# Kernel tuning notes

Measured on AMD Instinct MI355X. Metric: run time of the kernel, lower is better.

The kernel has to match this reference:

```python
import jax, jax.numpy as jnp
import numpy as np
import math

B, S, D, H = 64, 575, 256, 8
FF = 4 * D
EPS = 1e-5
DILATIONS = (1, 2, 4)


def _ln(x, g, b):
    mu = jnp.mean(x, axis=-1, keepdims=True)
    var = jnp.var(x, axis=-1, keepdims=True)
    return (x - mu) * jax.lax.rsqrt(var + EPS) * g + b


def setup_inputs() -> dict:
    key = jax.random.key(0)
    ks = jax.random.split(key, 8)
    w = lambda k, shape: jax.random.normal(k, shape, jnp.float32) * 0.02
    return {
        'state': jax.random.normal(ks[0], (B, S, D), jnp.float32),
        'conv_w': w(ks[1], (3, D, D, 3, 3)),
        'conv_b': jnp.zeros((3, D), jnp.float32),
        'qkv_w': w(ks[2], (3 * D, D)),
        'qkv_b': jnp.zeros((3 * D,), jnp.float32),
        'o_w': w(ks[3], (D, D)),
        'o_b': jnp.zeros((D,), jnp.float32),
        'attn_bias': w(ks[4], (H, S, S)),
        'ffp_w': w(ks[5], (FF, D)),
        'ffp_b': jnp.zeros((FF,), jnp.float32),
        'ffg_w': w(ks[6], (FF, D)),
        'ffg_b': jnp.zeros((FF,), jnp.float32),
        'ffo_w': w(ks[7], (D, FF)),
        'ffo_b': jnp.zeros((D,), jnp.float32),
        'n1_g': jnp.ones((D,), jnp.float32), 'n1_b': jnp.zeros((D,), jnp.float32),
        'n2_g': jnp.ones((D,), jnp.float32), 'n2_b': jnp.zeros((D,), jnp.float32),
        'n3_g': jnp.ones((D,), jnp.float32), 'n3_b': jnp.zeros((D,), jnp.float32),
    }


def _forward(state, conv_w, conv_b, qkv_w, qkv_b, o_w, o_b, attn_bias,
             ffp_w, ffp_b, ffg_w, ffg_b, ffo_w, ffo_b,
             n1_g, n1_b, n2_g, n2_b, n3_g, n3_b):
    b, s, d = state.shape
    h = attn_bias.shape[0]
    hd = d // h
    spatial = int(round(math.sqrt(s + 1)))  # grid_size + 1; spatial^2 == s+1 here

    # --- multi-scale dilated conv mixing ---
    pad = jnp.zeros((b, 1, d), state.dtype)
    h2d = jnp.concatenate([pad, state], axis=1)            # (B, S+1, D)
    h2d = jnp.transpose(h2d, (0, 2, 1)).reshape(b, d, spatial, spatial)
    conv_sum = 0.0
    for i, dil in enumerate(DILATIONS):
        y = jax.lax.conv_general_dilated(
            h2d, conv_w[i], window_strides=(1, 1),
            padding=[(dil, dil), (dil, dil)], rhs_dilation=(dil, dil),
            dimension_numbers=('NCHW', 'OIHW', 'NCHW'))
        conv_sum = conv_sum + y + conv_b[i][None, :, None, None]
    h_flat = jnp.transpose(conv_sum.reshape(b, d, -1), (0, 2, 1))  # (B, S+1, D)
    hmix = h_flat[:, 1:, :]

    state = _ln(state + hmix, n1_g, n1_b)

    # --- self-attention with learned per-head pair bias ---
    qkv = state @ qkv_w.T + qkv_b                          # (B, S, 3D)
    q, k, v = jnp.split(qkv, 3, axis=-1)
    # NOTE: replicate torch's reshape (no transpose): (B,S,D) -> (B,H,S,hd)
    q = q.reshape(b, h, s, hd)
    k = k.reshape(b, h, s, hd)
    v = v.reshape(b, h, s, hd)
    scores = jnp.einsum('bhsd,bhtd->bhst', q, k) / math.sqrt(hd)
    scores = scores + attn_bias[None]
    attn = jax.nn.softmax(scores, axis=-1)
    out = jnp.einsum('bhst,bhtd->bhsd', attn, v)
    out = jnp.transpose(out, (0, 2, 1, 3)).reshape(b, s, d)

    state = _ln(state + out @ o_w.T + o_b, n2_g, n2_b)

    # --- gated feed-forward ---
    proj = state @ ffp_w.T + ffp_b
    gate = jax.nn.sigmoid(state @ ffg_w.T + ffg_b)
    ff = (proj * gate) @ ffo_w.T + ffo_b
    return _ln(state + ff, n3_g, n3_b)


def reference(state, conv_w, conv_b, qkv_w, qkv_b, o_w, o_b, attn_bias,
              ffp_w, ffp_b, ffg_w, ffg_b, ffo_w, ffo_b,
              n1_g, n1_b, n2_g, n2_b, n3_g, n3_b):
    return _forward(state, conv_w, conv_b, qkv_w, qkv_b, o_w, o_b, attn_bias,
                    ffp_w, ffp_b, ffg_w, ffg_b, ffo_w, ffo_b,
                    n1_g, n1_b, n2_g, n2_b, n3_g, n3_b)
```

## Files before the change

kernel.cpp:

```cpp
#include <hip/hip_runtime.h>
#include <hip/hip_bf16.h>
#include <cstdio>


typedef __attribute__((ext_vector_type(8))) short s8v;
typedef __attribute__((ext_vector_type(4))) float f32x4;
typedef unsigned short u16;

constexpr int kB = 64, kS = 575, kD = 256, kH = 8, kP = 576, kFF = 1024;
constexpr int kRows = kB * kS;
constexpr float kEps = 1e-5f;
constexpr float kScale = 0.17677669529663687f;
constexpr size_t kPdStride = 9420800;

__device__ __forceinline__ u16 f2b(float f) {
  __hip_bfloat16 h = __float2bfloat16(f);
  return *reinterpret_cast<u16*>(&h);
}
__device__ __forceinline__ void unpack2(unsigned int w, float& lo, float& hi) {
  union { float f; unsigned int u; } a, b;
  a.u = w << 16;
  b.u = w & 0xffff0000u;
  lo = a.f;
  hi = b.f;
}

__device__ __forceinline__ void gll16(const void* g, void* l) {
  __builtin_amdgcn_global_load_lds((const __attribute__((address_space(1))) void*)g,
                                   (__attribute__((address_space(3))) void*)l, 16, 0, 0);
}

__global__ void k_pack_convw(const float* __restrict__ cw, u16* __restrict__ wc) {
  int idx = blockIdx.x * 256 + threadIdx.x;
  if (idx >= 27 * kD * kD) return;
  int ci = idx & 255;
  int co = (idx >> 8) & 255;
  int tap = idx >> 16;
  int i = tap / 9, r = tap - i * 9;
  int ky = r / 3, kx = r - ky * 3;
  wc[idx] = f2b(cw[(((size_t)(i * kD + co) * kD + ci) * 3 + ky) * 3 + kx]);
}

__global__ void k_tobf16(const float* __restrict__ in, u16* __restrict__ out, int n) {
  int i = blockIdx.x * 256 + threadIdx.x;
  if (i < n) out[i] = f2b(in[i]);
}

__global__ void k_make_x0(const float* __restrict__ state, u16* __restrict__ x0,
                          u16* __restrict__ zrow) {
  int bp = blockIdx.x;
  int c = threadIdx.x;
  if (bp == kB * kP) { zrow[c] = 0; return; }
  int p = bp % kP;
  int b = bp / kP;
  float v = (p == 0) ? 0.f : state[((size_t)(b * kS + p - 1)) * kD + c];
  x0[(size_t)bp * kD + c] = f2b(v);
}

__global__ __launch_bounds__(256) void k_gemm(const u16* __restrict__ A,
                                              const u16* __restrict__ Bw,
                                              const float* __restrict__ bias,
                                              u16* __restrict__ Cb,
                                              int M, int N, int K) {
  __shared__ u16 As[2][8192];
  __shared__ u16 Bs[2][8192];
  const int t = threadIdx.x;
  const int wave = t >> 6, lane = t & 63;
  const int wm = wave >> 1, wn = wave & 1;
  const int lr = lane & 15, lk = lane >> 4;
  const int m0 = blockIdx.x * 128, n0 = blockIdx.y * 128;
  const int lrow = lane >> 3;
  const int swzk = ((lane & 7) ^ lrow) * 8;
  const u16 *ga[4], *gb[4];
#pragma unroll
  for (int i = 0; i < 4; ++i) {
    int r = 8 * wave + lrow + 32 * i;
    int ra = m0 + r;
    if (ra > M - 1) ra = M - 1;
    ga[i] = A + (size_t)ra * K + swzk;
    gb[i] = Bw + (size_t)(n0 + r) * K + swzk;
  }
  auto stage = [&](int kt, int buf) {
#pragma unroll
    for (int i = 0; i < 4; ++i) {
      gll16(ga[i] + kt, &As[buf][i * 2048 + wave * 512]);
      gll16(gb[i] + kt, &Bs[buf][i * 2048 + wave * 512]);
    }
  };
  f32x4 acc[4][4] = {};
  stage(0, 0);
  __syncthreads();
  const int NT = K >> 6;
  for (int s = 0; s < NT; ++s) {
    const int cur = s & 1;
    if (s + 1 < NT) stage((s + 1) << 6, cur ^ 1);
    s8v af[2][4], bfr[2][4];
#pragma unroll
    for (int kk = 0; kk < 2; ++kk)
#pragma unroll
      for (int i = 0; i < 4; ++i) {
        const int rA = wm * 64 + i * 16 + lr;
        const int rB = wn * 64 + i * 16 + lr;
        af[kk][i] = *(const s8v*)(&As[cur][rA * 64 + ((kk * 32 + lk * 8) ^ ((rA & 7) << 3))]);
        bfr[kk][i] = *(const s8v*)(&Bs[cur][rB * 64 + ((kk * 32 + lk * 8) ^ ((rB & 7) << 3))]);
      }
#pragma unroll
    for (int kk = 0; kk < 2; ++kk)
#pragma unroll
      for (int i = 0; i < 4; ++i)
#pragma unroll
        for (int j = 0; j < 4; ++j)
          acc[i][j] = __builtin_amdgcn_mfma_f32_16x16x32_bf16(af[kk][i], bfr[kk][j], acc[i][j], 0, 0, 0);
    __syncthreads();
  }
#pragma unroll
  for (int i = 0; i < 4; ++i) {
    const int rbase = m0 + wm * 64 + i * 16 + lk * 4;
#pragma unroll
    for (int j = 0; j < 4; ++j) {
      const int col = n0 + wn * 64 + j * 16 + lr;
      const float bv = bias[col];
#pragma unroll
      for (int q = 0; q < 4; ++q) {
        int r = rbase + q;
        if (r < M) Cb[(size_t)r * N + col] = f2b(acc[i][j][q] + bv);
      }
    }
  }
}

__global__ __launch_bounds__(256) void k_ff1(const u16* __restrict__ A,
                                             const u16* __restrict__ Wf,
                                             const float* __restrict__ pb,
                                             const float* __restrict__ gb,
                                             u16* __restrict__ H, int M) {
  __shared__ u16 As[2][4096];
  __shared__ u16 Bp[2][4096];
  __shared__ u16 Bg[2][4096];
  const int t = threadIdx.x;
  const int wave = t >> 6;
  const int wm = wave >> 1, wn = wave & 1;
  const int lr = t & 15, lk = (t & 63) >> 4;
  const int m0 = blockIdx.x * 128, n0 = blockIdx.y * 128;
  int ra = m0 + (t >> 2);
  int rb = ra + 64;
  if (ra > M - 1) ra = M - 1;
  if (rb > M - 1) rb = M - 1;
  const int koff = (((t & 3) ^ ((t >> 2) & 3)) * 8);
  const u16* gA0 = A + (size_t)ra * kD + koff;
  const u16* gA1 = A + (size_t)rb * kD + koff;
  const u16* gP0 = Wf + (size_t)(n0 + (t >> 2)) * kD + koff;
  const u16* gP1 = gP0 + (size_t)64 * kD;
  const u16* gG0 = gP0 + (size_t)1024 * kD;
  const u16* gG1 = gP1 + (size_t)1024 * kD;
  auto stage = [&](int kt, int buf) {
    gll16(gA0 + kt, &As[buf][wave * 512]);
    gll16(gA1 + kt, &As[buf][2048 + wave * 512]);
    gll16(gP0 + kt, &Bp[buf][wave * 512]);
    gll16(gP1 + kt, &Bp[buf][2048 + wave * 512]);
    gll16(gG0 + kt, &Bg[buf][wave * 512]);
    gll16(gG1 + kt, &Bg[buf][2048 + wave * 512]);
  };
  f32x4 ap[4][4] = {};
  f32x4 ag[4][4] = {};
  stage(0, 0);
  __syncthreads();
  for (int s = 0; s < 8; ++s) {
    const int cur = s & 1;
    if (s < 7) stage((s + 1) << 5, cur ^ 1);
    s8v af[4], bp4[4], bg4[4];
#pragma unroll
    for (int i = 0; i < 4; ++i) {
      const int rA = wm * 64 + i * 16 + lr;
      const int rB = wn * 64 + i * 16 + lr;
      const int oA = rA * 32 + ((lk * 8) ^ ((rA & 3) << 3));
      const int oB = rB * 32 + ((lk * 8) ^ ((rB & 3) << 3));
      af[i] = *(const s8v*)(&As[cur][oA]);
      bp4[i] = *(const s8v*)(&Bp[cur][oB]);
      bg4[i] = *(const s8v*)(&Bg[cur][oB]);
    }
#pragma unroll
    for (int i = 0; i < 4; ++i)
#pragma unroll
      for (int j = 0; j < 4; ++j) {
        ap[i][j] = __builtin_amdgcn_mfma_f32_16x16x32_bf16(af[i], bp4[j], ap[i][j], 0, 0, 0);
        ag[i][j] = __builtin_amdgcn_mfma_f32_16x16x32_bf16(af[i], bg4[j], ag[i][j], 0, 0, 0);
      }
    __syncthreads();
  }
#pragma unroll
  for (int i = 0; i < 4; ++i) {
    const int rbase = m0 + wm * 64 + i * 16 + lk * 4;
#pragma unroll
    for (int j = 0; j < 4; ++j) {
      const int col = n0 + wn * 64 + j * 16 + lr;
      const float pbv = pb[col], gbv = gb[col];
#pragma unroll
      for (int q = 0; q < 4; ++q) {
        int r = rbase + q;
        if (r < M) {
          float p = ap[i][j][q] + pbv;
          float g = ag[i][j][q] + gbv;
          H[(size_t)r * kFF + col] = f2b(p * (1.f / (1.f + __expf(-g))));
        }
      }
    }
  }
}

__global__ __launch_bounds__(256) void k_conv(const u16* __restrict__ X0,
                                              const u16* __restrict__ zrow,
                                              const u16* __restrict__ Wc,
                                              const float* __restrict__ cb,
                                              u16* __restrict__ pd) {
  __shared__ u16 As[2][8192];
  __shared__ u16 Bs[2][8192];
  const int t = threadIdx.x;
  const int wave = t >> 6, lane = t & 63;
  const int wm = wave >> 1, wn = wave & 1;
  const int lr = lane & 15, lk = lane >> 4;
  const int m0 = blockIdx.x * 128;
  const int n0 = blockIdx.y * 128;
  const int di = blockIdx.z;
  const int dil = 1 << di;
  const int lrow = lane >> 3;
  const int swzk = ((lane & 7) ^ lrow) * 8;
  const u16* Wd = Wc + ((size_t)di * 9 << 16);
  int py[4], px[4];
  const u16* xrow[4];
  const u16* gw[4];
#pragma unroll
  for (int i = 0; i < 4; ++i) {
    int r = 8 * wave + lrow + 32 * i;
    int m = m0 + r;
    int bbv = m / 576;
    int p = m - bbv * 576;
    py[i] = p / 24;
    px[i] = p - py[i] * 24;
    xrow[i] = X0 + (((size_t)(bbv * kP)) << 8) + swzk;
    gw[i] = Wd + (size_t)(n0 + r) * kD + swzk;
  }
  const u16* S0[4];
  const u16* S1[4];
  auto csrc = [&](const u16** dst, int dyv, int dxv) {
#pragma unroll
    for (int i = 0; i < 4; ++i) {
      const int ny = py[i] + dyv, nx = px[i] + dxv;
      const bool v = ((unsigned)ny < 24u) & ((unsigned)nx < 24u);
      dst[i] = v ? xrow[i] + ((ny * 24 + nx) << 8) : zrow + swzk;
    }
  };
  auto stage = [&](const u16* const* S, size_t woff, int kc, int buf) {
#pragma unroll
    for (int i = 0; i < 4; ++i) {
      gll16(S[i] + kc, &As[buf][i * 2048 + wave * 512]);
      gll16(gw[i] + woff + kc, &Bs[buf][i * 2048 + wave * 512]);
    }
  };
  f32x4 acc[4][4] = {};
  csrc(S0, -dil, -dil);
  stage(S0, 0, 0, 0);
  stage(S0, 0, 64, 1);
  for (int tap = 0; tap < 9; ++tap) {
    if (tap < 8) {
      const int tn = tap + 1;
      csrc(S1, (tn / 3 - 1) * dil, (tn % 3 - 1) * dil);
    }
    const size_t woff = (size_t)tap << 16;
#pragma unroll
    for (int c = 0; c < 4; ++c) {
      const int buf = c & 1;
      if (c == 3 && tap == 8) {
        asm volatile("s_waitcnt vmcnt(0)" ::: "memory");
      } else {
        asm volatile("s_waitcnt vmcnt(8)" ::: "memory");
      }
      __builtin_amdgcn_s_barrier();
      s8v af[2][4], bfr[2][4];
#pragma unroll
      for (int kk = 0; kk < 2; ++kk)
#pragma unroll
        for (int ii = 0; ii < 4; ++ii) {
          const int rA = wm * 64 + ii * 16 + lr;
          const int rB = wn * 64 + ii * 16 + lr;
          af[kk][ii] = *(const s8v*)(&As[buf][rA * 64 + ((kk * 32 + lk * 8) ^ ((rA & 7) << 3))]);
          bfr[kk][ii] = *(const s8v*)(&Bs[buf][rB * 64 + ((kk * 32 + lk * 8) ^ ((rB & 7) << 3))]);
        }
#pragma unroll
      for (int kk = 0; kk < 2; ++kk)
#pragma unroll
        for (int ii = 0; ii < 4; ++ii)
#pragma unroll
          for (int jj = 0; jj < 4; ++jj)
            acc[ii][jj] = __builtin_amdgcn_mfma_f32_16x16x32_bf16(af[kk][ii], bfr[kk][jj], acc[ii][jj], 0, 0, 0);
      __builtin_amdgcn_s_barrier();
      if (c == 0) {
        stage(S0, woff, 128, buf);
      } else if (c == 1) {
        stage(S0, woff, 192, buf);
      } else if (c == 2) {
        if (tap < 8) stage(S1, woff + 65536, 0, buf);
      } else {
        if (tap < 8) stage(S1, woff + 65536, 64, buf);
      }
    }
#pragma unroll
    for (int i = 0; i < 4; ++i) S0[i] = S1[i];
  }
  u16* pdo = pd + (size_t)di * kPdStride;
#pragma unroll
  for (int i2 = 0; i2 < 4; ++i2) {
    const int mbase = m0 + wm * 64 + i2 * 16 + lk * 4;
#pragma unroll
    for (int j = 0; j < 4; ++j) {
      const int col = n0 + wn * 64 + j * 16 + lr;
      const float bv = cb[di * kD + col];
#pragma unroll
      for (int q = 0; q < 4; ++q) {
        const int m = mbase + q;
        const int b2 = m / 576;
        const int p = m - b2 * 576;
        if (p >= 1)
          pdo[((size_t)(b2 * kS + p - 1) << 8) + col] = f2b(acc[i2][j][q] + bv);
      }
    }
  }
}

__global__ __launch_bounds__(256) void k_attn2(const u16* __restrict__ qkv,
                                               const float* __restrict__ bias,
                                               u16* __restrict__ outp) {
  __shared__ u16 KsS[2][2048];
  __shared__ u16 VtS[2][2048];
  __shared__ u16 PsS[4][1024];
  const int qt = blockIdx.x, h = blockIdx.y, b = blockIdx.z;
  const int tid = threadIdx.x;
  const int w = tid >> 6, lane = tid & 63;
  const int lg = lane >> 4, lr = lane & 15;
  const int q0 = qt * 64;
  const int qrow_a = q0 + w * 16 + lr;
  const int qrow_ac = qrow_a < kS ? qrow_a : kS - 1;
  s8v qf;
  {
    int F = h * (kS * 32) + qrow_ac * 32 + lg * 8;
    qf = *(const s8v*)(qkv + ((size_t)(b * kS + (F >> 8))) * 768 + (F & 255));
  }
  const int trel = tid >> 2;
  const int dcol = (tid & 3) * 8;
  float mrun[4], lsum[4];
#pragma unroll
  for (int r = 0; r < 4; ++r) { mrun[r] = -1e30f; lsum[r] = 0.f; }
  f32x4 o0 = {0.f, 0.f, 0.f, 0.f}, o1 = {0.f, 0.f, 0.f, 0.f};
  const f32x4 zf = {0.f, 0.f, 0.f, 0.f};
  const int qrow_s = q0 + w * 16 + lg * 4;
  const size_t kvrowbase = (size_t)(b * kS) * 768;

  for (int kt = 0; kt < 9; ++kt) {
    const int t0 = kt * 64;
    const int buf = kt & 1;
    {
      const int tg = t0 + trel;
      const bool tv = tg < kS;
      const int tcl = tv ? tg : kS - 1;
      const int Fk = h * (kS * 32) + tcl * 32 + dcol;
      const u16* kp = qkv + kvrowbase + (size_t)(Fk >> 8) * 768 + 256 + (Fk & 255);
      uint4 kd = {0, 0, 0, 0}, vd = {0, 0, 0, 0};
      if (tv) {
        kd = *(const uint4*)kp;
        vd = *(const uint4*)(kp + 256);
      }
      *(uint4*)&KsS[buf][trel * 32 + (dcol ^ ((trel & 3) << 3))] = kd;
      union { uint4 u4; u16 us[8]; } vu;
      vu.u4 = vd;
#pragma unroll
      for (int j = 0; j < 8; ++j) {
        const int d = dcol + j;
        VtS[buf][d * 64 + (trel ^ ((d & 7) << 3))] = vu.us[j];
      }
    }
    float bv[4][4];
#pragma unroll
    for (int r = 0; r < 4; ++r) {
      const int qr = qrow_s + r;
      const float* bp = bias + ((size_t)h * kS + (qr < kS ? qr : kS - 1)) * kS;
#pragma unroll
      for (int j = 0; j < 4; ++j) {
        const int tg = t0 + j * 16 + lr;
        bv[j][r] = (tg < kS) ? bp[tg] : -1e30f;
      }
    }
    __syncthreads();
    f32x4 sc[4];
#pragma unroll
    for (int j = 0; j < 4; ++j) {
      const int krow = j * 16 + lr;
      s8v kf = *(const s8v*)&KsS[buf][krow * 32 + ((lg * 8) ^ ((krow & 3) << 3))];
      sc[j] = __builtin_amdgcn_mfma_f32_16x16x32_bf16(qf, kf, zf, 0, 0, 0);
    }
#pragma unroll
    for (int r = 0; r < 4; ++r) {
      float s4[4];
      float sm = -1e30f;
#pragma unroll
      for (int j = 0; j < 4; ++j) {
        s4[j] = fmaf(sc[j][r], kScale, bv[j][r]);
        sm = fmaxf(sm, s4[j]);
      }
      sm = fmaxf(sm, __shfl_xor(sm, 1));
      sm = fmaxf(sm, __shfl_xor(sm, 2));
      sm = fmaxf(sm, __shfl_xor(sm, 4));
      sm = fmaxf(sm, __shfl_xor(sm, 8));
      const float nm = fmaxf(mrun[r], sm);
      const float corr = __expf(mrun[r] - nm);
      mrun[r] = nm;
      float psum = 0.f;
      const int prow = lg * 4 + r;
#pragma unroll
      for (int j = 0; j < 4; ++j) {
        const float p = __expf(s4[j] - nm);
        psum += p;
        PsS[w][prow * 64 + ((j * 16 + lr) ^ ((prow & 7) << 3))] = f2b(p);
      }
      lsum[r] = fmaf(lsum[r], corr, psum);
      o0[r] *= corr;
      o1[r] *= corr;
    }
#pragma unroll
    for (int c = 0; c < 2; ++c) {
      const int pcol = c * 32 + lg * 8;
      s8v pf = *(const s8v*)&PsS[w][lr * 64 + (pcol ^ ((lr & 7) << 3))];
      s8v vf0 = *(const s8v*)&VtS[buf][lr * 64 + (pcol ^ ((lr & 7) << 3))];
      s8v vf1 = *(const s8v*)&VtS[buf][(16 + lr) * 64 + (pcol ^ (((16 + lr) & 7) << 3))];
      o0 = __builtin_amdgcn_mfma_f32_16x16x32_bf16(pf, vf0, o0, 0, 0, 0);
      o1 = __builtin_amdgcn_mfma_f32_16x16x32_bf16(pf, vf1, o1, 0, 0, 0);
    }
  }
#pragma unroll
  for (int r = 0; r < 4; ++r) {
    float lt = lsum[r];
    lt += __shfl_xor(lt, 1);
    lt += __shfl_xor(lt, 2);
    lt += __shfl_xor(lt, 4);
    lt += __shfl_xor(lt, 8);
    const float inv = 1.f / lt;
    const int qr = qrow_s + r;
    if (qr < kS) {
      u16* op = outp + ((size_t)(b * kS + qr)) * kD + h * 32;
      op[lr] = f2b(o0[r] * inv);
      op[16 + lr] = f2b(o1[r] * inv);
    }
  }
}

__global__ __launch_bounds__(256) void k_add_ln(const float* __restrict__ xa,
                                                const u16* __restrict__ xb,
                                                const float* __restrict__ g,
                                                const float* __restrict__ be,
                                                float* __restrict__ of, u16* __restrict__ ob) {
  const int wave = threadIdx.x >> 6, lane = threadIdx.x & 63;
  const int row = blockIdx.x * 4 + wave;
  const float4 a = ((const float4*)(xa + (size_t)row * kD))[lane];
  uint2 bw = ((const uint2*)(xb + (size_t)row * kD))[lane];
  float b0, b1, b2, b3;
  unpack2(bw.x, b0, b1);
  unpack2(bw.y, b2, b3);
  float x0 = a.x + b0, x1 = a.y + b1, x2 = a.z + b2, x3 = a.w + b3;
  float sum = x0 + x1 + x2 + x3;
  float sq = fmaf(x0, x0, fmaf(x1, x1, fmaf(x2, x2, x3 * x3)));
  for (int off = 1; off < 64; off <<= 1) {
    sum += __shfl_xor(sum, off);
    sq += __shfl_xor(sq, off);
  }
  const float mean = sum * (1.f / 256.f);
  const float var = sq * (1.f / 256.f) - mean * mean;
  const float rs = rsqrtf(var + kEps);
  const float4 gg = ((const float4*)g)[lane];
  const float4 bt = ((const float4*)be)[lane];
  float y0 = (x0 - mean) * rs * gg.x + bt.x;
  float y1 = (x1 - mean) * rs * gg.y + bt.y;
  float y2 = (x2 - mean) * rs * gg.z + bt.z;
  float y3 = (x3 - mean) * rs * gg.w + bt.w;
  float4 yo = {y0, y1, y2, y3};
  ((float4*)(of + (size_t)row * kD))[lane] = yo;
  if (ob) {
    u16* po = ob + (size_t)row * kD + lane * 4;
    po[0] = f2b(y0); po[1] = f2b(y1); po[2] = f2b(y2); po[3] = f2b(y3);
  }
}

__global__ __launch_bounds__(256) void k_add_ln3(const float* __restrict__ xa,
                                                 const u16* __restrict__ pa,
                                                 const u16* __restrict__ pbq,
                                                 const u16* __restrict__ pc,
                                                 const float* __restrict__ g,
                                                 const float* __restrict__ be,
                                                 float* __restrict__ of, u16* __restrict__ ob) {
  const int wave = threadIdx.x >> 6, lane = threadIdx.x & 63;
  const int row = blockIdx.x * 4 + wave;
  const size_t base = (size_t)row * kD;
  const float4 a = ((const float4*)(xa + base))[lane];
  uint2 w0 = ((const uint2*)(pa + base))[lane];
  uint2 w1 = ((const uint2*)(pbq + base))[lane];
  uint2 w2 = ((const uint2*)(pc + base))[lane];
  float a0, a1, a2, a3, c0, c1, c2, c3, d0, d1, d2, d3;
  unpack2(w0.x, a0, a1); unpack2(w0.y, a2, a3);
  unpack2(w1.x, c0, c1); unpack2(w1.y, c2, c3);
  unpack2(w2.x, d0, d1); unpack2(w2.y, d2, d3);
  float x0 = a.x + a0 + c0 + d0, x1 = a.y + a1 + c1 + d1;
  float x2 = a.z + a2 + c2 + d2, x3 = a.w + a3 + c3 + d3;
  float sum = x0 + x1 + x2 + x3;
  float sq = fmaf(x0, x0, fmaf(x1, x1, fmaf(x2, x2, x3 * x3)));
  for (int off = 1; off < 64; off <<= 1) {
    sum += __shfl_xor(sum, off);
    sq += __shfl_xor(sq, off);
  }
  const float mean = sum * (1.f / 256.f);
  const float var = sq * (1.f / 256.f) - mean * mean;
  const float rs = rsqrtf(var + kEps);
  const float4 gg = ((const float4*)g)[lane];
  const float4 bt = ((const float4*)be)[lane];
  float y0 = (x0 - mean) * rs * gg.x + bt.x;
  float y1 = (x1 - mean) * rs * gg.y + bt.y;
  float y2 = (x2 - mean) * rs * gg.z + bt.z;
  float y3 = (x3 - mean) * rs * gg.w + bt.w;
  float4 yo = {y0, y1, y2, y3};
  ((float4*)(of + base))[lane] = yo;
  u16* po = ob + base + lane * 4;
  po[0] = f2b(y0); po[1] = f2b(y1); po[2] = f2b(y2); po[3] = f2b(y3);
}

extern "C" void kernel_launch(void* const* d_in, const int* in_sizes, int n_in,
                              void* d_out, int out_size, void* d_ws, size_t ws_size,
                              hipStream_t stream) {
  const float* state = (const float*)d_in[0];
  const float* conv_w = (const float*)d_in[1];
  const float* conv_b = (const float*)d_in[2];
  const float* qkv_w = (const float*)d_in[3];
  const float* qkv_b = (const float*)d_in[4];
  const float* o_w = (const float*)d_in[5];
  const float* o_b = (const float*)d_in[6];
  const float* attn_bias = (const float*)d_in[7];
  const float* ffp_w = (const float*)d_in[8];
  const float* ffp_b = (const float*)d_in[9];
  const float* ffg_w = (const float*)d_in[10];
  const float* ffg_b = (const float*)d_in[11];
  const float* ffo_w = (const float*)d_in[12];
  const float* ffo_b = (const float*)d_in[13];
  const float* n1_g = (const float*)d_in[14];
  const float* n1_b = (const float*)d_in[15];
  const float* n2_g = (const float*)d_in[16];
  const float* n2_b = (const float*)d_in[17];
  const float* n3_g = (const float*)d_in[18];
  const float* n3_b = (const float*)d_in[19];

  constexpr size_t kWsNeed = 137527296;
  if (ws_size < kWsNeed) {
    fprintf(stderr, "[kernel] ws_size=%zu < need=%zu\n", ws_size, kWsNeed);
    return;
  }
  char* ws = (char*)d_ws;
  u16* Wc = (u16*)(ws + 0);
  u16* Wqkv = (u16*)(ws + 3538944);
  u16* Wo = (u16*)(ws + 3932160);
  u16* Wff = (u16*)(ws + 4063232);
  u16* Wffo = (u16*)(ws + 5111808);
  float* stF = (float*)(ws + 5636096);
  u16* stB = (u16*)(ws + 43319296);
  char* S4 = ws + 62160896;
  u16* X0 = (u16*)(ws + 5636096);
  u16* zrow = (u16*)(ws + 43319296);
  u16* pd = (u16*)S4;
  u16* qkvb = (u16*)S4;
  u16* attnout = (u16*)(S4 + 56524800);
  u16* oprojb = (u16*)S4;
  u16* ffh = (u16*)S4;
  float* outp = (float*)d_out;

  k_pack_convw<<<6912, 256, 0, stream>>>(conv_w, Wc);
  k_tobf16<<<768, 256, 0, stream>>>(qkv_w, Wqkv, 768 * 256);
  k_tobf16<<<256, 256, 0, stream>>>(o_w, Wo, 256 * 256);
  k_tobf16<<<1024, 256, 0, stream>>>(ffp_w, Wff, 1024 * 256);
  k_tobf16<<<1024, 256, 0, stream>>>(ffg_w, Wff + 1024 * 256, 1024 * 256);
  k_tobf16<<<1024, 256, 0, stream>>>(ffo_w, Wffo, 256 * 1024);
  k_make_x0<<<kB * kP + 1, 256, 0, stream>>>(state, X0, zrow);

  k_conv<<<dim3(288, 2, 3), 256, 0, stream>>>(X0, zrow, Wc, conv_b, pd);
  k_add_ln3<<<kRows / 4, 256, 0, stream>>>(state, pd, pd + kPdStride, pd + 2 * kPdStride,
                                           n1_g, n1_b, stF, stB);

  k_gemm<<<dim3(288, 6), 256, 0, stream>>>(stB, Wqkv, qkv_b, qkvb, kRows, 768, 256);
  k_attn2<<<dim3(9, kH, kB), 256, 0, stream>>>(qkvb, attn_bias, attnout);
  k_gemm<<<dim3(288, 2), 256, 0, stream>>>(attnout, Wo, o_b, oprojb, kRows, 256, 256);
  k_add_ln<<<kRows / 4, 256, 0, stream>>>(stF, oprojb, n2_g, n2_b, stF, stB);

  k_ff1<<<dim3(288, 8), 256, 0, stream>>>(stB, Wff, ffp_b, ffg_b, ffh, kRows);
  k_gemm<<<dim3(288, 2), 256, 0, stream>>>(ffh, Wffo, ffo_b, stB, kRows, 256, 1024);
  k_add_ln<<<kRows / 4, 256, 0, stream>>>(stF, stB, n3_g, n3_b, outp, nullptr);
}
```

Baseline: 517.8 us.

## Deepen GEMM prefetch with explicit vmcnt waits and register-prefetch attention K/V

The two GEMM kernels now issue two stages of async global-to-LDS loads up front. Each iteration waits on vmcnt for only the current buffer before a raw barrier, and the refill of a buffer is issued two tiles ahead right after it has been consumed. This keeps more memory traffic in flight and drops the full __syncthreads drain. The attention kernel prefetches the next tile's K/V and bias into registers while the current tile computes, which adds register pressure. The hardcoded vmcnt counts depend on each stage issuing exactly 8 or 6 loads.

```diff
diff --git a/kernel.cpp b/kernel.cpp
--- a/kernel.cpp
+++ b/kernel.cpp
@@ -88,12 +88,16 @@
     }
   };
   f32x4 acc[4][4] = {};
+  const int NT = K >> 6;
   stage(0, 0);
-  __syncthreads();
-  const int NT = K >> 6;
+  if (NT > 1) stage(64, 1);
   for (int s = 0; s < NT; ++s) {
     const int cur = s & 1;
-    if (s + 1 < NT) stage((s + 1) << 6, cur ^ 1);
+    if (s + 1 < NT)
+      asm volatile("s_waitcnt vmcnt(8)" ::: "memory");
+    else
+      asm volatile("s_waitcnt vmcnt(0)" ::: "memory");
+    __builtin_amdgcn_s_barrier();
     s8v af[2][4], bfr[2][4];
 #pragma unroll
     for (int kk = 0; kk < 2; ++kk)
@@ -111,7 +115,8 @@
 #pragma unroll
         for (int j = 0; j < 4; ++j)
           acc[i][j] = __builtin_amdgcn_mfma_f32_16x16x32_bf16(af[kk][i], bfr[kk][j], acc[i][j], 0, 0, 0);
-    __syncthreads();
+    __builtin_amdgcn_s_barrier();
+    if (s + 2 < NT) stage((s + 2) << 6, cur);
   }
 #pragma unroll
   for (int i = 0; i < 4; ++i) {
@@ -164,10 +169,14 @@
   f32x4 ap[4][4] = {};
   f32x4 ag[4][4] = {};
   stage(0, 0);
-  __syncthreads();
+  stage(32, 1);
   for (int s = 0; s < 8; ++s) {
     const int cur = s & 1;
-    if (s < 7) stage((s + 1) << 5, cur ^ 1);
+    if (s < 7)
+      asm volatile("s_waitcnt vmcnt(6)" ::: "memory");
+    else
+      asm volatile("s_waitcnt vmcnt(0)" ::: "memory");
+    __builtin_amdgcn_s_barrier();
     s8v af[4], bp4[4], bg4[4];
 #pragma unroll
     for (int i = 0; i < 4; ++i) {
@@ -186,7 +195,8 @@
         ap[i][j] = __builtin_amdgcn_mfma_f32_16x16x32_bf16(af[i], bp4[j], ap[i][j], 0, 0, 0);
         ag[i][j] = __builtin_amdgcn_mfma_f32_16x16x32_bf16(af[i], bg4[j], ag[i][j], 0, 0, 0);
       }
-    __syncthreads();
+    __builtin_amdgcn_s_barrier();
+    if (s < 6) stage((s + 2) << 5, cur);
   }
 #pragma unroll
   for (int i = 0; i < 4; ++i) {
@@ -354,22 +364,43 @@
   const f32x4 zf = {0.f, 0.f, 0.f, 0.f};
   const int qrow_s = q0 + w * 16 + lg * 4;
   const size_t kvrowbase = (size_t)(b * kS) * 768;
+  const float* bp0 = bias + (size_t)h * kS * kS;
+
+  uint4 kd, vd;
+  float bvn[4][4];
+  auto load_kv = [&](int kt) {
+    const int tg = kt * 64 + trel;
+    const bool tv = tg < kS;
+    const int tcl = tv ? tg : kS - 1;
+    const int Fk = h * (kS * 32) + tcl * 32 + dcol;
+    const u16* kp = qkv + kvrowbase + (size_t)(Fk >> 8) * 768 + 256 + (Fk & 255);
+    kd = make_uint4(0, 0, 0, 0);
+    vd = make_uint4(0, 0, 0, 0);
+    if (tv) {
+      kd = *(const uint4*)kp;
+      vd = *(const uint4*)(kp + 256);
+    }
+  };
+  auto load_bias = [&](int kt) {
+    const int t0k = kt * 64;
+#pragma unroll
+    for (int r = 0; r < 4; ++r) {
+      const int qr = qrow_s + r;
+      const float* bp = bp0 + (size_t)(qr < kS ? qr : kS - 1) * kS;
+#pragma unroll
+      for (int j = 0; j < 4; ++j) {
+        const int tg = t0k + j * 16 + lr;
+        bvn[j][r] = (tg < kS) ? bp[tg] : -1e30f;
+      }
+    }
+  };
+  load_kv(0);
+  load_bias(0);
 
   for (int kt = 0; kt < 9; ++kt) {
-    const int t0 = kt * 64;
     const int buf = kt & 1;
+    *(uint4*)&KsS[buf][trel * 32 + (dcol ^ ((trel & 3) << 3))] = kd;
     {
-      const int tg = t0 + trel;
-      const bool tv = tg < kS;
-      const int tcl = tv ? tg : kS - 1;
-      const int Fk = h * (kS * 32) + tcl * 32 + dcol;
-      const u16* kp = qkv + kvrowbase + (size_t)(Fk >> 8) * 768 + 256 + (Fk & 255);
-      uint4 kd = {0, 0, 0, 0}, vd = {0, 0, 0, 0};
-      if (tv) {
-        kd = *(const uint4*)kp;
-        vd = *(const uint4*)(kp + 256);
-      }
-      *(uint4*)&KsS[buf][trel * 32 + (dcol ^ ((trel & 3) << 3))] = kd;
       union { uint4 u4; u16 us[8]; } vu;
       vu.u4 = vd;
 #pragma unroll
@@ -380,16 +411,14 @@
     }
     float bv[4][4];
 #pragma unroll
-    for (int r = 0; r < 4; ++r) {
-      const int qr = qrow_s + r;
-      const float* bp = bias + ((size_t)h * kS + (qr < kS ? qr : kS - 1)) * kS;
-#pragma unroll
-      for (int j = 0; j < 4; ++j) {
-        const int tg = t0 + j * 16 + lr;
-        bv[j][r] = (tg < kS) ? bp[tg] : -1e30f;
-      }
-    }
+    for (int r = 0; r < 4; ++r)
+#pragma unroll
+      for (int j = 0; j < 4; ++j) bv[j][r] = bvn[j][r];
     __syncthreads();
+    if (kt < 8) {
+      load_kv(kt + 1);
+      load_bias(kt + 1);
+    }
     f32x4 sc[4];
 #pragma unroll
     for (int j = 0; j < 4; ++j) {
```

Result: slower. 545.6 us (+5.4%).
